# Kernel optimization log

Hardware: AMD Instinct MI355X
Metric: run time of the kernel (lower is better)

## Reference

```python
import jax, jax.numpy as jnp
import numpy as np

T, H, I, E, K, G, TG = 8192, 2048, 1024, 64, 8, 8, 4
ROUTED_SCALE = 2.5


def setup_inputs() -> dict:
    key = jax.random.key(0)
    ks = jax.random.split(key, 7)
    s = 0.02  # weight init scale
    return {
        "hidden_states": jax.random.normal(ks[0], (T, H), jnp.float32),
        "gate_w": jax.random.normal(ks[1], (E, H), jnp.float32) * s,
        "e_bias": jax.random.normal(ks[2], (E,), jnp.float32) * s,
        "w_gate_up": jax.random.normal(ks[3], (E, H, 2 * I), jnp.float32) * s,
        "w_down": jax.random.normal(ks[4], (E, I, H), jnp.float32) * s,
        "shared_gate_up": jax.random.normal(ks[5], (H, 2 * I), jnp.float32) * s,
        "shared_down": jax.random.normal(ks[6], (I, H), jnp.float32) * s,
    }


def silu_and_mul(x):
    g, u = jnp.split(x, 2, axis=-1)
    return jax.nn.silu(g) * u


def grouped_topk(router_logits, e_bias):
    # sigmoid scoring with e_score_correction_bias (DeepSeek-V3 / GLM4-MoE style)
    scores = jax.nn.sigmoid(router_logits)            # [T, E]
    scores_for_choice = scores + e_bias[None, :]
    # group score = sum of top-2 biased scores in each group
    grp = scores_for_choice.reshape(-1, G, E // G)
    group_scores = jax.lax.top_k(grp, 2)[0].sum(-1)   # [T, G]
    _, gidx = jax.lax.top_k(group_scores, TG)         # [T, TG]
    tok = jnp.arange(scores.shape[0])[:, None]
    group_mask = jnp.zeros_like(group_scores, dtype=bool).at[tok, gidx].set(True)
    expert_mask = jnp.repeat(group_mask, E // G, axis=-1)  # [T, E]
    masked = jnp.where(expert_mask, scores_for_choice, -jnp.inf)
    _, topk_ids = jax.lax.top_k(masked, K)            # [T, K]
    # combine weights come from the *unbiased* sigmoid scores
    topk_w = jnp.take_along_axis(scores, topk_ids, axis=-1)
    topk_w = topk_w / jnp.sum(topk_w, axis=-1, keepdims=True)  # renormalize
    return topk_w, topk_ids


def reference(hidden_states, gate_w, e_bias, w_gate_up, w_down,
              shared_gate_up, shared_down):
    x = hidden_states                                  # [T, H]
    # gate runs in fp32
    router_logits = x.astype(jnp.float32) @ gate_w.T   # [T, E]
    topk_w, topk_ids = grouped_topk(router_logits, e_bias)

    # shared expert MLP
    shared_out = silu_and_mul(x @ shared_gate_up) @ shared_down  # [T, H]

    # dense [T, E] combine matrix (top-k sparse in values)
    tok = jnp.arange(x.shape[0])[:, None]
    route = jnp.zeros((x.shape[0], E), x.dtype).at[tok, topk_ids].set(
        topk_w.astype(x.dtype))

    # grouped expert GEMMs via scan over experts (bounds peak memory)
    def body(acc, params):
        w1, w2, rw = params                            # [H,2I], [I,H], [T]
        y = silu_and_mul(x @ w1) @ w2                  # [T, H]
        return acc + rw[:, None] * y, None

    acc0 = jnp.zeros_like(x)
    routed_out, _ = jax.lax.scan(body, acc0, (w_gate_up, w_down, route.T))

    return routed_out * ROUTED_SCALE + shared_out
```

## Files before the change

kernel.cpp:

```cpp
#include <hip/hip_runtime.h>
#include <stdint.h>

#define T_TOK 8192
#define HDIM  2048
#define IDIM  1024
#define NEXP  64
#define KTOP  8
#define TGRP  4
#define TKTOT (T_TOK*KTOP)
#define MAXITEMS 12288
#define RSCALE 2.5f

typedef __attribute__((ext_vector_type(8))) short short8;
typedef __attribute__((ext_vector_type(4))) float f32x4;

#define VMCNT(n) asm volatile("s_waitcnt vmcnt(" #n ")" ::: "memory")
#define BARRIER() asm volatile("s_barrier" ::: "memory")

__device__ __forceinline__ float bf2f(uint16_t u) {
    union { unsigned i; float f; } v; v.i = ((unsigned)u) << 16; return v.f;
}
__device__ __forceinline__ uint16_t f2bf(float f) {
    union { float f; unsigned i; } v; v.f = f;
    unsigned r = (v.i + 0x7FFFu + ((v.i >> 16) & 1u)) >> 16;
    return (uint16_t)r;
}
__device__ __forceinline__ void gload_lds16(const void* g, void* l) {
    __builtin_amdgcn_global_load_lds(
        (const __attribute__((address_space(1))) void*)g,
        (__attribute__((address_space(3))) void*)l, 16, 0, 0);
}
__device__ __forceinline__ int imin(int a, int b) { return a < b ? a : b; }

__global__ __launch_bounds__(256) void k_router(
    const float* __restrict__ x, const float* __restrict__ gw,
    const float* __restrict__ ebias,
    int* __restrict__ topk_ids, float* __restrict__ topk_w,
    int* __restrict__ counts)
{
    __shared__ float xs[16][132];
    __shared__ float wsb[64][133];
    __shared__ float sc[16][65];
    __shared__ float su[16][65];
    const int tid = threadIdx.x;
    const int e = tid & 63;
    const int tg = tid >> 6;
    const long tblk = (long)blockIdx.x * 16;

    float acc0 = 0.f, acc1 = 0.f, acc2 = 0.f, acc3 = 0.f;
    for (int ch = 0; ch < 16; ++ch) {
        const int h0 = ch << 7;
        for (int i = tid; i < 512; i += 256) {
            int r = i >> 5, c4 = (i & 31) << 2;
            float4 v = *(const float4*)(x + (tblk + r) * HDIM + h0 + c4);
            *(float4*)&xs[r][c4] = v;
        }
        for (int i = tid; i < 8192; i += 256) {
            int r = i >> 7, c = i & 127;
            wsb[r][c] = gw[(long)r * HDIM + h0 + c];
        }
        __syncthreads();
        #pragma unroll 8
        for (int hh = 0; hh < 128; ++hh) {
            float wv = wsb[e][hh];
            acc0 += xs[tg][hh] * wv;
            acc1 += xs[tg + 4][hh] * wv;
            acc2 += xs[tg + 8][hh] * wv;
            acc3 += xs[tg + 12][hh] * wv;
        }
        __syncthreads();
    }
    const float be = ebias[e];
    {
        float s;
        s = 1.f / (1.f + expf(-acc0)); su[tg][e] = s;      sc[tg][e] = s + be;
        s = 1.f / (1.f + expf(-acc1)); su[tg + 4][e] = s;  sc[tg + 4][e] = s + be;
        s = 1.f / (1.f + expf(-acc2)); su[tg + 8][e] = s;  sc[tg + 8][e] = s + be;
        s = 1.f / (1.f + expf(-acc3)); su[tg + 12][e] = s; sc[tg + 12][e] = s + be;
    }
    __syncthreads();
    if (tid < 16) {
        const int t = tid;
        float gs[8];
        #pragma unroll
        for (int g = 0; g < 8; ++g) {
            float m1 = -1e30f, m2 = -1e30f;
            #pragma unroll
            for (int j = 0; j < 8; ++j) {
                float v = sc[t][g * 8 + j];
                if (v > m1) { m2 = m1; m1 = v; } else if (v > m2) { m2 = v; }
            }
            gs[g] = m1 + m2;
        }
        int selmask = 0;
        #pragma unroll
        for (int it = 0; it < TGRP; ++it) {
            float best = -1e30f; int bg = 0;
            #pragma unroll
            for (int g = 0; g < 8; ++g)
                if (!((selmask >> g) & 1) && gs[g] > best) { best = gs[g]; bg = g; }
            selmask |= (1 << bg);
        }
        unsigned long long chosen = 0ull;
        int ids[KTOP]; float wv[KTOP]; float wsum = 0.f;
        #pragma unroll
        for (int it = 0; it < KTOP; ++it) {
            float best = -1e30f; int bi = 0;
            for (int ee = 0; ee < 64; ++ee) {
                if (((selmask >> (ee >> 3)) & 1) && !((chosen >> ee) & 1ull)) {
                    float v = sc[t][ee];
                    if (v > best) { best = v; bi = ee; }
                }
            }
            chosen |= (1ull << bi);
            ids[it] = bi; wv[it] = su[t][bi]; wsum += wv[it];
        }
        const float inv = 1.f / wsum;
        #pragma unroll
        for (int k = 0; k < KTOP; ++k) {
            topk_ids[(tblk + t) * KTOP + k] = ids[k];
            topk_w[(tblk + t) * KTOP + k] = wv[k] * inv;
            atomicAdd(&counts[ids[k]], 1);
        }
    }
}

__global__ __launch_bounds__(64) void k_scan3(
    const int* __restrict__ counts, int* offsets, int* cursor,
    int* __restrict__ it_r0, int* __restrict__ it_end,
    int* __restrict__ it_e, int* __restrict__ it_n0, int* __restrict__ nitems)
{
    const int e = threadIdx.x;
    const int c = counts[e];
    int pre = c;
    #pragma unroll
    for (int d = 1; d < 64; d <<= 1) {
        int v = __shfl_up(pre, d, 64);
        if (e >= d) pre += v;
    }
    const int offE = pre - c;
    offsets[e] = offE; cursor[e] = offE;
    const int ntl = (c + 127) >> 7;
    int ipre = ntl;
    #pragma unroll
    for (int d = 1; d < 64; d <<= 1) {
        int v = __shfl_up(ipre, d, 64);
        if (e >= d) ipre += v;
    }
    const int ibase = (ipre - ntl) * 16;
    for (int p = 0; p < 16; ++p)
        for (int t = 0; t < ntl; ++t) {
            int idx = ibase + p * ntl + t;
            it_r0[idx] = offE + t * 128;
            it_end[idx] = offE + c;
            it_e[idx] = e;
            it_n0[idx] = p << 7;
        }
    if (e == 63) *nitems = ibase + ntl * 16;
}

__global__ __launch_bounds__(256) void k_scatter(
    const int* __restrict__ topk_ids, int* cursor,
    int* __restrict__ perm_token, int* __restrict__ slot_of)
{
    int i = blockIdx.x * 256 + threadIdx.x;
    if (i >= TKTOT) return;
    int e = topk_ids[i];
    int pos = atomicAdd(&cursor[e], 1);
    perm_token[pos] = i >> 3;
    slot_of[i] = pos;
}

__global__ __launch_bounds__(256) void k_cvt_bf16(
    const float* __restrict__ in, uint16_t* __restrict__ outp, long n4)
{
    long i = (long)blockIdx.x * 256 + threadIdx.x;
    if (i >= n4) return;
    float4 v = *(const float4*)(in + i * 4);
    uint64_t pk = (uint64_t)f2bf(v.x) | ((uint64_t)f2bf(v.y) << 16)
                | ((uint64_t)f2bf(v.z) << 32) | ((uint64_t)f2bf(v.w) << 48);
    *(uint64_t*)(outp + i * 4) = pk;
}

template<bool INTER>
__global__ __launch_bounds__(256) void k_transpose2(
    const float* __restrict__ src, uint16_t* __restrict__ dst,
    int R, int C, long sStride, long dStride)
{
    __shared__ float tile[64][65];
    const int c0 = blockIdx.x << 6, r0 = blockIdx.y << 6, s = blockIdx.z;
    const float* S = src + (long)s * sStride;
    uint16_t* D = dst + (long)s * dStride;
    const int lc = (threadIdx.x & 15) << 2;
    const int lr = threadIdx.x >> 4;
    #pragma unroll
    for (int p = 0; p < 4; ++p) {
        int y = lr + p * 16;
        float4 v = *(const float4*)(S + (long)(r0 + y) * C + c0 + lc);
        tile[y][lc] = v.x; tile[y][lc + 1] = v.y;
        tile[y][lc + 2] = v.z; tile[y][lc + 3] = v.w;
    }
    __syncthreads();
    const int wc = threadIdx.x >> 3;
    const int wx = (threadIdx.x & 7) << 3;
    #pragma unroll
    for (int p = 0; p < 2; ++p) {
        int c = wc + p * 32;
        short8 v;
        #pragma unroll
        for (int j = 0; j < 8; ++j) v[j] = (short)f2bf(tile[wx + j][c]);
        int cg = c0 + c;
        int rd = INTER ? (((cg & (IDIM - 1)) << 1) + (cg >> 10)) : cg;
        *(short8*)(D + (long)rd * R + r0 + wx) = v;
    }
}

template<bool GATEUP, bool ROUTED>
__global__ __launch_bounds__(256, 2) void k_gemm7(
    const uint16_t* __restrict__ A, const uint16_t* __restrict__ Bw,
    void* __restrict__ OutP,
    const int* __restrict__ perm_token,
    const int* __restrict__ it_r0, const int* __restrict__ it_end,
    const int* __restrict__ it_e, const int* __restrict__ it_n0,
    const int* __restrict__ nitems, int* __restrict__ qcur,
    int Kd, long expStride)
{
    __shared__ char ldsb[4 * 16384];
    __shared__ int s_item;
    const int tid = threadIdx.x, lane = tid & 63, wid = tid >> 6;
    const int wm = wid >> 1, wn = wid & 1;

    const int rchunk = lane >> 2;
    const int swzS = ((lane & 3) ^ ((lane >> 3) & 3)) << 3;
    const int swzR = ((lane >> 4) ^ ((lane >> 1) & 3)) << 4;
    const int aoff = (wm * 64 + (lane & 15)) * 64 + swzR;
    const int boff = (wn * 64 + (lane & 15)) * 64 + swzR;
    const int dst0 = (wid * 2) * 1024;
    const int dst1 = (wid * 2 + 1) * 1024;

    const int nKt = Kd >> 5;
    const int NI = ROUTED ? nitems[0] : 0;

    for (;;) {
        int row0, end, n0; long eoff;
        if (ROUTED) {
            __syncthreads();
            if (tid == 0) s_item = atomicAdd(qcur, 1);
            __syncthreads();
            const int it = s_item;
            if (it >= NI) break;
            row0 = it_r0[it]; end = it_end[it]; n0 = it_n0[it];
            eoff = (long)it_e[it] * expStride;
        } else {
            row0 = (int)(blockIdx.x >> 4) << 7;
            end = row0 + 128;
            n0 = (int)(blockIdx.x & 15) << 7;
            eoff = 0;
        }

        const uint16_t *pa0, *pa1, *pb0, *pb1;
        {
            int r0l = wid * 32 + rchunk;
            int r1l = r0l + 16;
            int ra0 = row0 + r0l, ra1 = row0 + r1l;
            if (ROUTED) { ra0 = imin(ra0, end - 1); ra1 = imin(ra1, end - 1); }
            long ga0 = (GATEUP && ROUTED) ? (long)perm_token[ra0] : (long)ra0;
            long ga1 = (GATEUP && ROUTED) ? (long)perm_token[ra1] : (long)ra1;
            pa0 = A + ga0 * Kd + swzS;
            pa1 = A + ga1 * Kd + swzS;
            pb0 = Bw + eoff + (long)(n0 + r0l) * Kd + swzS;
            pb1 = Bw + eoff + (long)(n0 + r1l) * Kd + swzS;
        }

        f32x4 acc[4][4];
        #pragma unroll
        for (int f = 0; f < 4; ++f)
            #pragma unroll
            for (int g = 0; g < 4; ++g) { f32x4 z = {0.f,0.f,0.f,0.f}; acc[f][g] = z; }

        #pragma unroll
        for (int j = 0; j < 3; ++j) {
            char* bb = ldsb + j * 16384;
            gload_lds16(pa0 + (j << 5), bb + dst0);
            gload_lds16(pa1 + (j << 5), bb + dst1);
            gload_lds16(pb0 + (j << 5), bb + 8192 + dst0);
            gload_lds16(pb1 + (j << 5), bb + 8192 + dst1);
        }

        for (int kt = 0; kt < nKt; ++kt) {
            if (kt + 2 < nKt)      VMCNT(8);
            else if (kt + 1 < nKt) VMCNT(4);
            else                   VMCNT(0);
            BARRIER();
            const char* bb = ldsb + (kt & 3) * 16384;
            char* bs = ldsb + ((kt + 3) & 3) * 16384;
            short8 fa0 = *(const short8*)(bb + aoff);
            short8 fa1 = *(const short8*)(bb + aoff + 1024);
            short8 fa2 = *(const short8*)(bb + aoff + 2048);
            short8 fa3 = *(const short8*)(bb + aoff + 3072);
            short8 fb0 = *(const short8*)(bb + 8192 + boff);
            short8 fb1 = *(const short8*)(bb + 8192 + boff + 1024);
            short8 fb2 = *(const short8*)(bb + 8192 + boff + 2048);
            short8 fb3 = *(const short8*)(bb + 8192 + boff + 3072);
            if (kt + 3 < nKt) {
                gload_lds16(pa0 + ((kt + 3) << 5), bs + dst0);
                gload_lds16(pa1 + ((kt + 3) << 5), bs + dst1);
                gload_lds16(pb0 + ((kt + 3) << 5), bs + 8192 + dst0);
                gload_lds16(pb1 + ((kt + 3) << 5), bs + 8192 + dst1);
            }
            BARRIER();
            __builtin_amdgcn_s_setprio(1);
            acc[0][0] = __builtin_amdgcn_mfma_f32_16x16x32_bf16(fa0, fb0, acc[0][0], 0, 0, 0);
            acc[0][1] = __builtin_amdgcn_mfma_f32_16x16x32_bf16(fa0, fb1, acc[0][1], 0, 0, 0);
            acc[0][2] = __builtin_amdgcn_mfma_f32_16x16x32_bf16(fa0, fb2, acc[0][2], 0, 0, 0);
            acc[0][3] = __builtin_amdgcn_mfma_f32_16x16x32_bf16(fa0, fb3, acc[0][3], 0, 0, 0);
            acc[1][0] = __builtin_amdgcn_mfma_f32_16x16x32_bf16(fa1, fb0, acc[1][0], 0, 0, 0);
            acc[1][1] = __builtin_amdgcn_mfma_f32_16x16x32_bf16(fa1, fb1, acc[1][1], 0, 0, 0);
            acc[1][2] = __builtin_amdgcn_mfma_f32_16x16x32_bf16(fa1, fb2, acc[1][2], 0, 0, 0);
            acc[1][3] = __builtin_amdgcn_mfma_f32_16x16x32_bf16(fa1, fb3, acc[1][3], 0, 0, 0);
            acc[2][0] = __builtin_amdgcn_mfma_f32_16x16x32_bf16(fa2, fb0, acc[2][0], 0, 0, 0);
            acc[2][1] = __builtin_amdgcn_mfma_f32_16x16x32_bf16(fa2, fb1, acc[2][1], 0, 0, 0);
            acc[2][2] = __builtin_amdgcn_mfma_f32_16x16x32_bf16(fa2, fb2, acc[2][2], 0, 0, 0);
            acc[2][3] = __builtin_amdgcn_mfma_f32_16x16x32_bf16(fa2, fb3, acc[2][3], 0, 0, 0);
            acc[3][0] = __builtin_amdgcn_mfma_f32_16x16x32_bf16(fa3, fb0, acc[3][0], 0, 0, 0);
            acc[3][1] = __builtin_amdgcn_mfma_f32_16x16x32_bf16(fa3, fb1, acc[3][1], 0, 0, 0);
            acc[3][2] = __builtin_amdgcn_mfma_f32_16x16x32_bf16(fa3, fb2, acc[3][2], 0, 0, 0);
            acc[3][3] = __builtin_amdgcn_mfma_f32_16x16x32_bf16(fa3, fb3, acc[3][3], 0, 0, 0);
            __builtin_amdgcn_s_setprio(0);
        }

        const int colb = n0 + wn * 64 + (lane & 15);
        const int rowbase = row0 + wm * 64 + ((lane >> 4) << 2);
        if (GATEUP) {
            uint16_t* Oact = (uint16_t*)OutP;
            const bool evenl = ((lane & 1) == 0);
            #pragma unroll
            for (int f = 0; f < 4; ++f)
                #pragma unroll
                for (int g = 0; g < 4; ++g) {
                    f32x4 v = acc[f][g];
                    #pragma unroll
                    for (int r = 0; r < 4; ++r) {
                        float gg = v[r];
                        float uu = __shfl_xor(gg, 1, 64);
                        int row = rowbase + f * 16 + r;
                        if (evenl && (!ROUTED || row < end)) {
                            int jcol = (colb + g * 16) >> 1;
                            float sg = gg / (1.f + __expf(-gg));
                            Oact[(long)row * IDIM + jcol] = f2bf(sg * uu);
                        }
                    }
                }
        } else if (ROUTED) {
            uint16_t* Y = (uint16_t*)OutP;
            #pragma unroll
            for (int f = 0; f < 4; ++f)
                #pragma unroll
                for (int g = 0; g < 4; ++g) {
                    f32x4 v = acc[f][g];
                    #pragma unroll
                    for (int r = 0; r < 4; ++r) {
                        int row = rowbase + f * 16 + r;
                        if (row < end)
                            Y[(long)row * HDIM + colb + g * 16] = f2bf(v[r]);
                    }
                }
        } else {
            float* O = (float*)OutP;
            #pragma unroll
            for (int f = 0; f < 4; ++f)
                #pragma unroll
                for (int g = 0; g < 4; ++g) {
                    f32x4 v = acc[f][g];
                    #pragma unroll
                    for (int r = 0; r < 4; ++r) {
                        int row = rowbase + f * 16 + r;
                        O[(long)row * HDIM + colb + g * 16] = v[r];
                    }
                }
        }
        if (!ROUTED) break;
    }
}

__global__ __launch_bounds__(256) void k_combine(
    float* __restrict__ out, const uint16_t* __restrict__ ybuf,
    const int* __restrict__ slot_of, const float* __restrict__ topk_w)
{
    __shared__ int sl[KTOP];
    __shared__ float sw[KTOP];
    const int t = blockIdx.x, tid = threadIdx.x;
    if (tid < KTOP) {
        sl[tid] = slot_of[t * KTOP + tid];
        sw[tid] = topk_w[t * KTOP + tid] * RSCALE;
    }
    __syncthreads();
    const int h0 = tid << 3;
    float* orow = out + (long)t * HDIM + h0;
    float4 v0 = *(const float4*)(orow);
    float4 v1 = *(const float4*)(orow + 4);
    float a[8] = { v0.x, v0.y, v0.z, v0.w, v1.x, v1.y, v1.z, v1.w };
    #pragma unroll
    for (int k = 0; k < KTOP; ++k) {
        const uint16_t* yr = ybuf + (long)sl[k] * HDIM + h0;
        short8 y = *(const short8*)yr;
        float w = sw[k];
        #pragma unroll
        for (int j = 0; j < 8; ++j)
            a[j] += w * bf2f((uint16_t)y[j]);
    }
    v0.x = a[0]; v0.y = a[1]; v0.z = a[2]; v0.w = a[3];
    v1.x = a[4]; v1.y = a[5]; v1.z = a[6]; v1.w = a[7];
    *(float4*)(orow) = v0;
    *(float4*)(orow + 4) = v1;
}

extern "C" void kernel_launch(void* const* d_in, const int* in_sizes, int n_in,
                              void* d_out, int out_size, void* d_ws, size_t ws_size,
                              hipStream_t stream)
{
    const float* x  = (const float*)d_in[0];
    const float* gw = (const float*)d_in[1];
    const float* eb = (const float*)d_in[2];
    const float* w1 = (const float*)d_in[3];
    const float* w2 = (const float*)d_in[4];
    const float* s1 = (const float*)d_in[5];
    const float* s2 = (const float*)d_in[6];
    float* out = (float*)d_out;
    char* ws = (char*)d_ws;

    size_t off = 0;
    auto take = [&](size_t b) { size_t r = off; off += (b + 255) & ~(size_t)255; return r; };
    const size_t oXBF = take((size_t)T_TOK * HDIM * 2);
    const size_t oACT = take((size_t)TKTOT * IDIM * 2);
    const size_t oASH = take((size_t)T_TOK * IDIM * 2);
    const size_t oW1T = take((size_t)NEXP * 2048 * 2048 * 2);
    const size_t oW2T = take((size_t)NEXP * 2048 * 1024 * 2);
    const size_t oS1T = take((size_t)2048 * 2048 * 2);
    const size_t oS2T = take((size_t)2048 * 1024 * 2);
    const size_t oTKI = take((size_t)TKTOT * 4);
    const size_t oTKW = take((size_t)TKTOT * 4);
    const size_t oSLT = take((size_t)TKTOT * 4);
    const size_t oPRM = take((size_t)TKTOT * 4);
    const size_t oCTL = take(1024);
    const size_t oOFS = take(256);
    const size_t oCUR = take(256);
    const size_t oNT  = take(256);
    const size_t oIR  = take(MAXITEMS * 4);
    const size_t oIE  = take(MAXITEMS * 4);
    const size_t oIX  = take(MAXITEMS * 4);
    const size_t oIN  = take(MAXITEMS * 4);
    (void)ws_size; (void)in_sizes; (void)n_in; (void)out_size;

    uint16_t* xbf  = (uint16_t*)(ws + oXBF);
    uint16_t* act  = (uint16_t*)(ws + oACT);
    uint16_t* ash  = (uint16_t*)(ws + oASH);
    uint16_t* w1t  = (uint16_t*)(ws + oW1T);
    uint16_t* ybuf = (uint16_t*)(ws + oW1T);
    uint16_t* w2t  = (uint16_t*)(ws + oW2T);
    uint16_t* s1t  = (uint16_t*)(ws + oS1T);
    uint16_t* s2t  = (uint16_t*)(ws + oS2T);
    int*   tki  = (int*)(ws + oTKI);
    float* tkw  = (float*)(ws + oTKW);
    int*   slot = (int*)(ws + oSLT);
    int*   prm  = (int*)(ws + oPRM);
    int*   ctl  = (int*)(ws + oCTL);
    int*   ofs  = (int*)(ws + oOFS);
    int*   cur  = (int*)(ws + oCUR);
    int*   nt   = (int*)(ws + oNT);
    int*   ir0  = (int*)(ws + oIR);
    int*   iend = (int*)(ws + oIE);
    int*   ie   = (int*)(ws + oIX);
    int*   in0  = (int*)(ws + oIN);

    hipMemsetAsync(ws + oCTL, 0, 1024, stream);

    k_router<<<T_TOK / 16, 256, 0, stream>>>(x, gw, eb, tki, tkw, ctl);
    k_scan3<<<1, 64, 0, stream>>>(ctl, ofs, cur, ir0, iend, ie, in0, nt);
    k_scatter<<<TKTOT / 256, 256, 0, stream>>>(tki, cur, prm, slot);

    k_cvt_bf16<<<(T_TOK * HDIM / 4 + 255) / 256, 256, 0, stream>>>(x, xbf, (long)T_TOK * HDIM / 4);
    k_transpose2<true ><<<dim3(32, 32, NEXP), 256, 0, stream>>>(w1, w1t, 2048, 2048,
        (long)2048 * 2048, (long)2048 * 2048);
    k_transpose2<false><<<dim3(32, 16, NEXP), 256, 0, stream>>>(w2, w2t, 1024, 2048,
        (long)1024 * 2048, (long)2048 * 1024);
    k_transpose2<true ><<<dim3(32, 32, 1), 256, 0, stream>>>(s1, s1t, 2048, 2048, 0, 0);
    k_transpose2<false><<<dim3(32, 16, 1), 256, 0, stream>>>(s2, s2t, 1024, 2048, 0, 0);

    k_gemm7<true, false><<<dim3(1024), 256, 0, stream>>>(
        xbf, s1t, ash, nullptr, nullptr, nullptr, nullptr, nullptr, nullptr, nullptr, 2048, 0);
    k_gemm7<true, true><<<dim3(512), 256, 0, stream>>>(
        xbf, w1t, act, prm, ir0, iend, ie, in0, nt, ctl + 64, 2048, (long)2048 * 2048);
    k_gemm7<false, false><<<dim3(1024), 256, 0, stream>>>(
        ash, s2t, out, nullptr, nullptr, nullptr, nullptr, nullptr, nullptr, nullptr, 1024, 0);
    k_gemm7<false, true><<<dim3(512), 256, 0, stream>>>(
        act, w2t, ybuf, nullptr, ir0, iend, ie, in0, nt, ctl + 65, 1024, (long)2048 * 1024);

    k_combine<<<T_TOK, 256, 0, stream>>>(out, ybuf, slot, tkw);
}
```

Baseline: 2.316 ms.

## Use 3-stage LDS pipeline for 3 blocks/CU and per-XCD work queues

The GEMM kernel's LDS ring shrinks from four stages to three with prefetch distance two, and launch bounds rise to three blocks per CU. The routed launches grow from 512 to 768 persistent blocks. Work items are reordered so the 16 N-tiles of each row tile are adjacent, and the item list is split into eight contiguous ranges, each with its own atomic cursor, chosen by blockIdx&7 (assumed to map to an XCD). The aim is higher occupancy, better L2 locality of A rows per XCD and less contention on one atomic. The cost is a shallower prefetch, which may expose memory latency, and no work stealing between the per-XCD queues, which risks load imbalance.

```diff
diff --git a/kernel.cpp b/kernel.cpp
--- a/kernel.cpp
+++ b/kernel.cpp
@@ -125,10 +125,11 @@
     }
 }
 
-__global__ __launch_bounds__(64) void k_scan3(
+__global__ __launch_bounds__(64) void k_scan5(
     const int* __restrict__ counts, int* offsets, int* cursor,
     int* __restrict__ it_r0, int* __restrict__ it_end,
-    int* __restrict__ it_e, int* __restrict__ it_n0, int* __restrict__ nitems)
+    int* __restrict__ it_e, int* __restrict__ it_n0,
+    int* __restrict__ nitems, int* __restrict__ qctl)
 {
     const int e = threadIdx.x;
     const int c = counts[e];
@@ -148,15 +149,23 @@
         if (e >= d) ipre += v;
     }
     const int ibase = (ipre - ntl) * 16;
-    for (int p = 0; p < 16; ++p)
-        for (int t = 0; t < ntl; ++t) {
-            int idx = ibase + p * ntl + t;
+    for (int t = 0; t < ntl; ++t)
+        for (int p = 0; p < 16; ++p) {
+            int idx = ibase + t * 16 + p;
             it_r0[idx] = offE + t * 128;
             it_end[idx] = offE + c;
             it_e[idx] = e;
             it_n0[idx] = p << 7;
         }
-    if (e == 63) *nitems = ibase + ntl * 16;
+    const int totTl = __shfl(ipre, 63, 64);
+    const int NI = totTl * 16;
+    if (e == 63) *nitems = NI;
+    if (e < 8) {
+        int s  = (int)(((long)e * NI) / 8);
+        int en = (int)(((long)(e + 1) * NI) / 8);
+        qctl[e] = s;       qctl[8 + e]  = en;
+        qctl[16 + e] = s;  qctl[24 + e] = en;
+    }
 }
 
 __global__ __launch_bounds__(256) void k_scatter(
@@ -216,7 +225,7 @@
 }
 
 template<bool GATEUP, bool ROUTED>
-__global__ __launch_bounds__(256, 2) void k_gemm7(
+__global__ __launch_bounds__(256, 3) void k_gemm10(
     const uint16_t* __restrict__ A, const uint16_t* __restrict__ Bw,
     void* __restrict__ OutP,
     const int* __restrict__ perm_token,
@@ -225,7 +234,7 @@
     const int* __restrict__ nitems, int* __restrict__ qcur,
     int Kd, long expStride)
 {
-    __shared__ char ldsb[4 * 16384];
+    __shared__ char ldsb[3 * 16384];
     __shared__ int s_item;
     const int tid = threadIdx.x, lane = tid & 63, wid = tid >> 6;
     const int wm = wid >> 1, wn = wid & 1;
@@ -239,16 +248,18 @@
     const int dst1 = (wid * 2 + 1) * 1024;
 
     const int nKt = Kd >> 5;
-    const int NI = ROUTED ? nitems[0] : 0;
+    const int xcd = (int)(blockIdx.x & 7);
+    const int myEnd = ROUTED ? qcur[8 + xcd] : 0;
+    int* myCur = qcur + xcd;
 
     for (;;) {
         int row0, end, n0; long eoff;
         if (ROUTED) {
             __syncthreads();
-            if (tid == 0) s_item = atomicAdd(qcur, 1);
+            if (tid == 0) s_item = atomicAdd(myCur, 1);
             __syncthreads();
             const int it = s_item;
-            if (it >= NI) break;
+            if (it >= myEnd) break;
             row0 = it_r0[it]; end = it_end[it]; n0 = it_n0[it];
             eoff = (long)it_e[it] * expStride;
         } else {
@@ -278,22 +289,22 @@
             #pragma unroll
             for (int g = 0; g < 4; ++g) { f32x4 z = {0.f,0.f,0.f,0.f}; acc[f][g] = z; }
 
-        #pragma unroll
-        for (int j = 0; j < 3; ++j) {
-            char* bb = ldsb + j * 16384;
-            gload_lds16(pa0 + (j << 5), bb + dst0);
-            gload_lds16(pa1 + (j << 5), bb + dst1);
-            gload_lds16(pb0 + (j << 5), bb + 8192 + dst0);
-            gload_lds16(pb1 + (j << 5), bb + 8192 + dst1);
-        }
-
+        gload_lds16(pa0, ldsb + dst0);
+        gload_lds16(pa1, ldsb + dst1);
+        gload_lds16(pb0, ldsb + 8192 + dst0);
+        gload_lds16(pb1, ldsb + 8192 + dst1);
+        gload_lds16(pa0 + 32, ldsb + 16384 + dst0);
+        gload_lds16(pa1 + 32, ldsb + 16384 + dst1);
+        gload_lds16(pb0 + 32, ldsb + 16384 + 8192 + dst0);
+        gload_lds16(pb1 + 32, ldsb + 16384 + 8192 + dst1);
+
+        int cur = 0, stg = 2;
         for (int kt = 0; kt < nKt; ++kt) {
-            if (kt + 2 < nKt)      VMCNT(8);
-            else if (kt + 1 < nKt) VMCNT(4);
-            else                   VMCNT(0);
+            if (kt + 1 < nKt) VMCNT(4);
+            else              VMCNT(0);
             BARRIER();
-            const char* bb = ldsb + (kt & 3) * 16384;
-            char* bs = ldsb + ((kt + 3) & 3) * 16384;
+            const char* bb = ldsb + cur * 16384;
+            char* bs = ldsb + stg * 16384;
             short8 fa0 = *(const short8*)(bb + aoff);
             short8 fa1 = *(const short8*)(bb + aoff + 1024);
             short8 fa2 = *(const short8*)(bb + aoff + 2048);
@@ -302,11 +313,11 @@
             short8 fb1 = *(const short8*)(bb + 8192 + boff + 1024);
             short8 fb2 = *(const short8*)(bb + 8192 + boff + 2048);
             short8 fb3 = *(const short8*)(bb + 8192 + boff + 3072);
-            if (kt + 3 < nKt) {
-                gload_lds16(pa0 + ((kt + 3) << 5), bs + dst0);
-                gload_lds16(pa1 + ((kt + 3) << 5), bs + dst1);
-                gload_lds16(pb0 + ((kt + 3) << 5), bs + 8192 + dst0);
-                gload_lds16(pb1 + ((kt + 3) << 5), bs + 8192 + dst1);
+            if (kt + 2 < nKt) {
+                gload_lds16(pa0 + ((kt + 2) << 5), bs + dst0);
+                gload_lds16(pa1 + ((kt + 2) << 5), bs + dst1);
+                gload_lds16(pb0 + ((kt + 2) << 5), bs + 8192 + dst0);
+                gload_lds16(pb1 + ((kt + 2) << 5), bs + 8192 + dst1);
             }
             BARRIER();
             __builtin_amdgcn_s_setprio(1);
@@ -327,6 +338,8 @@
             acc[3][2] = __builtin_amdgcn_mfma_f32_16x16x32_bf16(fa3, fb2, acc[3][2], 0, 0, 0);
             acc[3][3] = __builtin_amdgcn_mfma_f32_16x16x32_bf16(fa3, fb3, acc[3][3], 0, 0, 0);
             __builtin_amdgcn_s_setprio(0);
+            cur = (cur == 2) ? 0 : cur + 1;
+            stg = (stg == 2) ? 0 : stg + 1;
         }
 
         const int colb = n0 + wn * 64 + (lane & 15);
@@ -472,11 +485,12 @@
     int*   iend = (int*)(ws + oIE);
     int*   ie   = (int*)(ws + oIX);
     int*   in0  = (int*)(ws + oIN);
+    int*   qctl = ctl + 64;
 
     hipMemsetAsync(ws + oCTL, 0, 1024, stream);
 
     k_router<<<T_TOK / 16, 256, 0, stream>>>(x, gw, eb, tki, tkw, ctl);
-    k_scan3<<<1, 64, 0, stream>>>(ctl, ofs, cur, ir0, iend, ie, in0, nt);
+    k_scan5<<<1, 64, 0, stream>>>(ctl, ofs, cur, ir0, iend, ie, in0, nt, qctl);
     k_scatter<<<TKTOT / 256, 256, 0, stream>>>(tki, cur, prm, slot);
 
     k_cvt_bf16<<<(T_TOK * HDIM / 4 + 255) / 256, 256, 0, stream>>>(x, xbf, (long)T_TOK * HDIM / 4);
@@ -487,14 +501,14 @@
     k_transpose2<true ><<<dim3(32, 32, 1), 256, 0, stream>>>(s1, s1t, 2048, 2048, 0, 0);
     k_transpose2<false><<<dim3(32, 16, 1), 256, 0, stream>>>(s2, s2t, 1024, 2048, 0, 0);
 
-    k_gemm7<true, false><<<dim3(1024), 256, 0, stream>>>(
-        xbf, s1t, ash, nullptr, nullptr, nullptr, nullptr, nullptr, nullptr, nullptr, 2048, 0);
-    k_gemm7<true, true><<<dim3(512), 256, 0, stream>>>(
-        xbf, w1t, act, prm, ir0, iend, ie, in0, nt, ctl + 64, 2048, (long)2048 * 2048);
-    k_gemm7<false, false><<<dim3(1024), 256, 0, stream>>>(
-        ash, s2t, out, nullptr, nullptr, nullptr, nullptr, nullptr, nullptr, nullptr, 1024, 0);
-    k_gemm7<false, true><<<dim3(512), 256, 0, stream>>>(
-        act, w2t, ybuf, nullptr, ir0, iend, ie, in0, nt, ctl + 65, 1024, (long)2048 * 1024);
+    k_gemm10<true, false><<<dim3(1024), 256, 0, stream>>>(
+        xbf, s1t, ash, nullptr, nullptr, nullptr, nullptr, nullptr, nullptr, qctl, 2048, 0);
+    k_gemm10<true, true><<<dim3(768), 256, 0, stream>>>(
+        xbf, w1t, act, prm, ir0, iend, ie, in0, nt, qctl, 2048, (long)2048 * 2048);
+    k_gemm10<false, false><<<dim3(1024), 256, 0, stream>>>(
+        ash, s2t, out, nullptr, nullptr, nullptr, nullptr, nullptr, nullptr, qctl, 1024, 0);
+    k_gemm10<false, true><<<dim3(768), 256, 0, stream>>>(
+        act, w2t, ybuf, nullptr, ir0, iend, ie, in0, nt, qctl + 16, 1024, (long)2048 * 1024);
 
     k_combine<<<T_TOK, 256, 0, stream>>>(out, ybuf, slot, tkw);
 }
```

After: 2.253 ms. 1.03x faster.
